# Optimization experiments

Measured on AMD Instinct MI355X. Metric: run time of the kernel, lower is better.

## Reference

```python
import jax, jax.numpy as jnp
import numpy as np


def setup_inputs() -> dict:
    key = jax.random.key(0)
    ks = jax.random.split(key, 10)
    N1, N2, F, D, E = 50000, 50000, 1024, 128, 1000000
    s = 0.02
    return {
        "x_gene": jax.random.normal(ks[0], (N1, F), jnp.float32),
        "x_cell": jax.random.normal(ks[1], (N2, F), jnp.float32),
        "edge_label_index": jax.random.randint(ks[2], (2, E), 0, N1, jnp.int64 if jax.config.jax_enable_x64 else jnp.int32),
        "W1": jax.random.normal(ks[3], (F, D), jnp.float32) * s,
        "b1": jnp.zeros((D,), jnp.float32),
        "W2": jax.random.normal(ks[4], (F, D), jnp.float32) * s,
        "b2": jnp.zeros((D,), jnp.float32),
        "Wm1": jax.random.normal(ks[5], (2 * D, 64), jnp.float32) * s,
        "bm1": jnp.zeros((64,), jnp.float32),
        "Wm2": jax.random.normal(ks[6], (64, 32), jnp.float32) * s,
        "bm2": jnp.zeros((32,), jnp.float32),
        "Wm3": jax.random.normal(ks[7], (32, 1), jnp.float32) * s,
        "bm3": jnp.zeros((1,), jnp.float32),
    }


def reference(x_gene, x_cell, edge_label_index, W1, b1, W2, b2, Wm1, bm1, Wm2, bm2, Wm3, bm3):
    # Node-type linear projections (dropout is identity in eval mode)
    h1 = x_gene @ W1 + b1          # [N1, D]
    h2 = x_cell @ W2 + b2          # [N2, D]
    # Edge gather + concat
    ef = jnp.concatenate([h1[edge_label_index[0]], h2[edge_label_index[1]]], axis=-1)  # [E, 2D]
    # 3-layer MLP classifier
    h = jax.nn.relu(ef @ Wm1 + bm1)
    h = jax.nn.relu(h @ Wm2 + bm2)
    pred = (h @ Wm3 + bm3)[..., 0]  # squeeze(-1) -> [E]
    return pred
```

## Files before the change

### kernel.cpp

```cpp
#include <hip/hip_runtime.h>
#include <hip/hip_bf16.h>
#include <stdint.h>

typedef __attribute__((ext_vector_type(8))) short short8;
typedef __attribute__((ext_vector_type(4))) float float4v;

__device__ __forceinline__ float bf2f(uint16_t u) {
    union { uint32_t i; float f; } v; v.i = ((uint32_t)u) << 16; return v.f;
}
__device__ __forceinline__ uint16_t f2bf(float f) {
    union { float f; uint32_t i; } v; v.f = f;
    uint32_t x = v.i;
    uint32_t r = (x + 0x7fffu + ((x >> 16) & 1u)) >> 16;
    return (uint16_t)r;
}

__global__ __launch_bounds__(256) void precompute_kernel(
    const float* __restrict__ W1, const float* __restrict__ W2,
    const float* __restrict__ Wm1, const float* __restrict__ Wm2,
    const float* __restrict__ b1, const float* __restrict__ b2,
    const float* __restrict__ bm1,
    uint16_t* __restrict__ A1T, uint16_t* __restrict__ A2T,
    float* __restrict__ tbias, uint16_t* __restrict__ Wm2bfT)
{
    int b = blockIdx.x, t = threadIdx.x;
    if (b < 512) {
        int g   = b * 4 + (t >> 6);
        int mat = g >> 10;
        int f   = g & 1023;
        int n   = t & 63;
        const float* W    = mat ? W2 : W1;
        const float* wm   = Wm1 + mat * 128 * 64;
        const float* Wrow = W + (size_t)f * 128;
        float acc = 0.f;
        #pragma unroll 8
        for (int d = 0; d < 128; ++d)
            acc = fmaf(Wrow[d], wm[d * 64 + n], acc);
        (mat ? A2T : A1T)[(size_t)n * 1024 + f] = f2bf(acc);
    } else {
        int n  = t >> 3;
        int k0 = (t & 7) * 8;
        #pragma unroll
        for (int i = 0; i < 8; ++i)
            Wm2bfT[n * 64 + k0 + i] = f2bf(Wm2[(size_t)(k0 + i) * 32 + n]);
        if (t < 64) {
            float acc = bm1[t];
            for (int d = 0; d < 128; ++d) acc += b1[d] * Wm1[d * 64 + t];
            for (int d = 0; d < 128; ++d) acc += b2[d] * Wm1[(128 + d) * 64 + t];
            tbias[t] = acc;
        }
    }
}

__global__ __launch_bounds__(256) void gemm64_kernel(
    const float* __restrict__ X1, const float* __restrict__ X2,
    const uint16_t* __restrict__ A1T, const uint16_t* __restrict__ A2T,
    uint16_t* __restrict__ G1, uint16_t* __restrict__ G2, int M1, int M2)
{
    const int which = blockIdx.y;
    const float* __restrict__ X     = which ? X2  : X1;
    const uint16_t* __restrict__ BT = which ? A2T : A1T;
    uint16_t* __restrict__ G        = which ? G2  : G1;
    const int M = which ? M2 : M1;

    const int blockRow = blockIdx.x * 64;
    if (blockRow >= M) return;

    __shared__ uint16_t As[64 * 128];

    const int t    = threadIdx.x;
    const int wid  = t >> 6;
    const int lane = t & 63;
    const int m    = lane & 15;
    const int q    = lane >> 4;

    float4v acc[4];
    #pragma unroll
    for (int nt = 0; nt < 4; ++nt) acc[nt] = (float4v){0.f, 0.f, 0.f, 0.f};

    for (int kk = 0; kk < 8; ++kk) {
        float4 av0[4], av1[4];
        int    dstc[4];
        #pragma unroll
        for (int it = 0; it < 4; ++it) {
            int c   = it * 256 + t;
            int row = c >> 4, pc = c & 15;
            int lc  = pc ^ (row & 7);
            int grow = blockRow + row; if (grow >= M) grow = M - 1;
            const float4* src = (const float4*)(X + (size_t)grow * 1024 + kk * 128 + lc * 8);
            av0[it] = src[0];
            av1[it] = src[1];
            dstc[it] = c * 8;
        }
        __syncthreads();
        #pragma unroll
        for (int it = 0; it < 4; ++it) {
            uint4 pk;
            pk.x = (uint32_t)f2bf(av0[it].x) | ((uint32_t)f2bf(av0[it].y) << 16);
            pk.y = (uint32_t)f2bf(av0[it].z) | ((uint32_t)f2bf(av0[it].w) << 16);
            pk.z = (uint32_t)f2bf(av1[it].x) | ((uint32_t)f2bf(av1[it].y) << 16);
            pk.w = (uint32_t)f2bf(av1[it].z) | ((uint32_t)f2bf(av1[it].w) << 16);
            *(uint4*)(As + dstc[it]) = pk;
        }
        __syncthreads();

        #pragma unroll
        for (int p = 0; p < 4; ++p) {
            short8 af, bfr[4];
            int row = wid * 16 + m;
            int pc  = (p * 4 + q) ^ (row & 7);
            af = *(const short8*)(As + row * 128 + pc * 8);
            #pragma unroll
            for (int nt = 0; nt < 4; ++nt) {
                int n = nt * 16 + m;
                bfr[nt] = *(const short8*)(BT + (size_t)n * 1024 + kk * 128 + (p * 4 + q) * 8);
            }
            #pragma unroll
            for (int nt = 0; nt < 4; ++nt)
                acc[nt] = __builtin_amdgcn_mfma_f32_16x16x32_bf16(
                    af, bfr[nt], acc[nt], 0, 0, 0);
        }
    }

    #pragma unroll
    for (int reg = 0; reg < 4; ++reg) {
        int grow = blockRow + wid * 16 + q * 4 + reg;
        if (grow < M) {
            #pragma unroll
            for (int nt = 0; nt < 4; ++nt)
                G[(size_t)grow * 64 + nt * 16 + m] = f2bf(acc[nt][reg]);
        }
    }
}

__global__ __launch_bounds__(256) void edge_mlp_kernel(
    const uint16_t* __restrict__ g1, const uint16_t* __restrict__ g2,
    const float* __restrict__ tbias, const int* __restrict__ eidx,
    const uint16_t* __restrict__ Wm2bfT, const float* __restrict__ bm2,
    const float* __restrict__ Wm3, const float* __restrict__ bm3,
    float* __restrict__ out, int E)
{
    __shared__ uint16_t T[256 * 64];

    const int t    = threadIdx.x;
    const int wid  = t >> 6;
    const int lane = t & 63;
    const int m    = lane & 15;
    const int q    = lane >> 4;

    short8 bfrag[2][2];
    #pragma unroll
    for (int s = 0; s < 2; ++s)
        #pragma unroll
        for (int nt = 0; nt < 2; ++nt)
            bfrag[s][nt] = *(const short8*)(Wm2bfT + (nt * 16 + m) * 64 + s * 32 + q * 8);

    const float bm2a = bm2[m],      bm2b = bm2[16 + m];
    const float w3a  = Wm3[m],      w3b  = Wm3[16 + m];
    const float b3   = bm3[0];

    const int tileBase = blockIdx.x * 256;
    int e = tileBase + t; if (e >= E) e = E - 1;
    const int src = eidx[e];
    const int dst = eidx[E + e];
    const uint4* r1 = (const uint4*)(g1 + (size_t)src * 64);
    const uint4* r2 = (const uint4*)(g2 + (size_t)dst * 64);

    uint4 A[8], B[8];
    #pragma unroll
    for (int c = 0; c < 8; ++c) { A[c] = r1[c]; B[c] = r2[c]; }

    #pragma unroll
    for (int c = 0; c < 8; ++c) {
        uint32_t aw[4] = { A[c].x, A[c].y, A[c].z, A[c].w };
        uint32_t bw[4] = { B[c].x, B[c].y, B[c].z, B[c].w };
        uint32_t pw[4];
        #pragma unroll
        for (int h = 0; h < 4; ++h) {
            float alo, ahi, blo, bhi;
            { union { uint32_t i; float f; } v; v.i = aw[h] << 16;        alo = v.f; }
            { union { uint32_t i; float f; } v; v.i = aw[h] & 0xffff0000u; ahi = v.f; }
            { union { uint32_t i; float f; } v; v.i = bw[h] << 16;        blo = v.f; }
            { union { uint32_t i; float f; } v; v.i = bw[h] & 0xffff0000u; bhi = v.f; }
            float t0 = fmaxf(alo + blo + tbias[c * 8 + 2 * h],     0.f);
            float t1 = fmaxf(ahi + bhi + tbias[c * 8 + 2 * h + 1], 0.f);
            pw[h] = (uint32_t)f2bf(t0) | ((uint32_t)f2bf(t1) << 16);
        }
        uint4 pk; pk.x = pw[0]; pk.y = pw[1]; pk.z = pw[2]; pk.w = pw[3];
        int pc = c ^ (t & 7);
        *(uint4*)(T + t * 64 + pc * 8) = pk;
    }
    __syncthreads();

    float4v acc[4][2];
    #pragma unroll
    for (int r = 0; r < 4; ++r) {
        acc[r][0] = (float4v){0.f, 0.f, 0.f, 0.f};
        acc[r][1] = (float4v){0.f, 0.f, 0.f, 0.f};
    }
    #pragma unroll
    for (int r = 0; r < 4; ++r) {
        const int row = wid * 64 + r * 16 + m;
        #pragma unroll
        for (int s = 0; s < 2; ++s) {
            const int pc = (s * 4 + q) ^ (row & 7);
            short8 af = *(const short8*)(T + row * 64 + pc * 8);
            acc[r][0] = __builtin_amdgcn_mfma_f32_16x16x32_bf16(af, bfrag[s][0], acc[r][0], 0, 0, 0);
            acc[r][1] = __builtin_amdgcn_mfma_f32_16x16x32_bf16(af, bfrag[s][1], acc[r][1], 0, 0, 0);
        }
    }

    #pragma unroll
    for (int r = 0; r < 4; ++r) {
        #pragma unroll
        for (int reg = 0; reg < 4; ++reg) {
            float v0 = fmaxf(acc[r][0][reg] + bm2a, 0.f);
            float v1 = fmaxf(acc[r][1][reg] + bm2b, 0.f);
            float p  = fmaf(v0, w3a, v1 * w3b);
            p += __shfl_xor(p, 1);
            p += __shfl_xor(p, 2);
            p += __shfl_xor(p, 4);
            p += __shfl_xor(p, 8);
            int eo = tileBase + wid * 64 + r * 16 + q * 4 + reg;
            if (m == 0 && eo < E) out[eo] = p + b3;
        }
    }
}

extern "C" void kernel_launch(void* const* d_in, const int* in_sizes, int n_in,
                              void* d_out, int out_size, void* d_ws, size_t ws_size,
                              hipStream_t stream) {
    const float* x_gene = (const float*)d_in[0];
    const float* x_cell = (const float*)d_in[1];
    const int*   eidx   = (const int*)d_in[2];
    const float* W1  = (const float*)d_in[3];
    const float* b1  = (const float*)d_in[4];
    const float* W2  = (const float*)d_in[5];
    const float* b2  = (const float*)d_in[6];
    const float* Wm1 = (const float*)d_in[7];
    const float* bm1 = (const float*)d_in[8];
    const float* Wm2 = (const float*)d_in[9];
    const float* bm2 = (const float*)d_in[10];
    const float* Wm3 = (const float*)d_in[11];
    const float* bm3 = (const float*)d_in[12];

    const int M1 = in_sizes[0] / 1024;
    const int M2 = in_sizes[1] / 1024;
    const int E  = in_sizes[2] / 2;

    uint8_t* ws = (uint8_t*)d_ws;
    uint16_t* A1T    = (uint16_t*)(ws + 0);
    uint16_t* A2T    = (uint16_t*)(ws + 131072);
    float*    tbias  = (float*)(ws + 262144);
    uint16_t* Wm2bfT = (uint16_t*)(ws + 262400);
    uint16_t* G1     = (uint16_t*)(ws + 524288);
    size_t g1_bytes  = ((size_t)M1 * 64 * 2 + 127) & ~(size_t)127;
    uint16_t* G2     = (uint16_t*)(ws + 524288 + g1_bytes);

    precompute_kernel<<<513, 256, 0, stream>>>(
        W1, W2, Wm1, Wm2, b1, b2, bm1, A1T, A2T, tbias, Wm2bfT);

    int Mmax = M1 > M2 ? M1 : M2;
    dim3 ggrid((Mmax + 63) / 64, 2);
    gemm64_kernel<<<ggrid, 256, 0, stream>>>(x_gene, x_cell, A1T, A2T, G1, G2, M1, M2);

    edge_mlp_kernel<<<(E + 255) / 256, 256, 0, stream>>>(
        G1, G2, tbias, eidx, Wm2bfT, bm2, Wm3, bm3, (float*)d_out, E);
}
```

Before: 543.6 us.

## Pipeline GEMM input loads with async global-to-LDS triple buffering

```diff
diff --git a/kernel.cpp b/kernel.cpp
--- a/kernel.cpp
+++ b/kernel.cpp
@@ -5,9 +5,9 @@
 typedef __attribute__((ext_vector_type(8))) short short8;
 typedef __attribute__((ext_vector_type(4))) float float4v;
 
-__device__ __forceinline__ float bf2f(uint16_t u) {
-    union { uint32_t i; float f; } v; v.i = ((uint32_t)u) << 16; return v.f;
-}
+typedef const __attribute__((address_space(1))) uint32_t* gas_ptr;
+typedef __attribute__((address_space(3))) uint32_t*       las_ptr;
+
 __device__ __forceinline__ uint16_t f2bf(float f) {
     union { float f; uint32_t i; } v; v.f = f;
     uint32_t x = v.i;
@@ -52,7 +52,7 @@
     }
 }
 
-__global__ __launch_bounds__(256) void gemm64_kernel(
+__global__ __launch_bounds__(256, 3) void gemm64_kernel(
     const float* __restrict__ X1, const float* __restrict__ X2,
     const uint16_t* __restrict__ A1T, const uint16_t* __restrict__ A2T,
     uint16_t* __restrict__ G1, uint16_t* __restrict__ G2, int M1, int M2)
@@ -66,61 +66,94 @@
     const int blockRow = blockIdx.x * 64;
     if (blockRow >= M) return;
 
-    __shared__ uint16_t As[64 * 128];
+    __shared__ __align__(16) float As[3 * 64 * 64];
 
     const int t    = threadIdx.x;
     const int wid  = t >> 6;
     const int lane = t & 63;
     const int m    = lane & 15;
     const int q    = lane >> 4;
+    const int sblk = wid * 4;
+
+    const float *sa0, *sa1, *sa2, *sa3;
+    {
+        int r0 = (sblk + 0) * 4 + (lane >> 4);
+        int r1 = (sblk + 1) * 4 + (lane >> 4);
+        int r2 = (sblk + 2) * 4 + (lane >> 4);
+        int r3 = (sblk + 3) * 4 + (lane >> 4);
+        int g0 = blockRow + r0; if (g0 >= M) g0 = M - 1;
+        int g1 = blockRow + r1; if (g1 >= M) g1 = M - 1;
+        int g2 = blockRow + r2; if (g2 >= M) g2 = M - 1;
+        int g3 = blockRow + r3; if (g3 >= M) g3 = M - 1;
+        sa0 = X + (size_t)g0 * 1024 + (((lane & 15) ^ (r0 & 15)) * 4);
+        sa1 = X + (size_t)g1 * 1024 + (((lane & 15) ^ (r1 & 15)) * 4);
+        sa2 = X + (size_t)g2 * 1024 + (((lane & 15) ^ (r2 & 15)) * 4);
+        sa3 = X + (size_t)g3 * 1024 + (((lane & 15) ^ (r3 & 15)) * 4);
+    }
+
+#define STAGE(ii, tb)                                                          \
+    do {                                                                       \
+        __builtin_amdgcn_global_load_lds((gas_ptr)(sa0 + (ii) * 64),           \
+            (las_ptr)((tb) + (sblk + 0) * 256), 16, 0, 0);                     \
+        __builtin_amdgcn_global_load_lds((gas_ptr)(sa1 + (ii) * 64),           \
+            (las_ptr)((tb) + (sblk + 1) * 256), 16, 0, 0);                     \
+        __builtin_amdgcn_global_load_lds((gas_ptr)(sa2 + (ii) * 64),           \
+            (las_ptr)((tb) + (sblk + 2) * 256), 16, 0, 0);                     \
+        __builtin_amdgcn_global_load_lds((gas_ptr)(sa3 + (ii) * 64),           \
+            (las_ptr)((tb) + (sblk + 3) * 256), 16, 0, 0);                     \
+    } while (0)
 
     float4v acc[4];
     #pragma unroll
     for (int nt = 0; nt < 4; ++nt) acc[nt] = (float4v){0.f, 0.f, 0.f, 0.f};
 
-    for (int kk = 0; kk < 8; ++kk) {
-        float4 av0[4], av1[4];
-        int    dstc[4];
-        #pragma unroll
-        for (int it = 0; it < 4; ++it) {
-            int c   = it * 256 + t;
-            int row = c >> 4, pc = c & 15;
-            int lc  = pc ^ (row & 7);
-            int grow = blockRow + row; if (grow >= M) grow = M - 1;
-            const float4* src = (const float4*)(X + (size_t)grow * 1024 + kk * 128 + lc * 8);
-            av0[it] = src[0];
-            av1[it] = src[1];
-            dstc[it] = c * 8;
-        }
-        __syncthreads();
-        #pragma unroll
-        for (int it = 0; it < 4; ++it) {
-            uint4 pk;
-            pk.x = (uint32_t)f2bf(av0[it].x) | ((uint32_t)f2bf(av0[it].y) << 16);
-            pk.y = (uint32_t)f2bf(av0[it].z) | ((uint32_t)f2bf(av0[it].w) << 16);
-            pk.z = (uint32_t)f2bf(av1[it].x) | ((uint32_t)f2bf(av1[it].y) << 16);
-            pk.w = (uint32_t)f2bf(av1[it].z) | ((uint32_t)f2bf(av1[it].w) << 16);
-            *(uint4*)(As + dstc[it]) = pk;
-        }
-        __syncthreads();
-
-        #pragma unroll
-        for (int p = 0; p < 4; ++p) {
-            short8 af, bfr[4];
-            int row = wid * 16 + m;
-            int pc  = (p * 4 + q) ^ (row & 7);
-            af = *(const short8*)(As + row * 128 + pc * 8);
+    STAGE(0, As);
+    STAGE(1, As + 4096);
+
+    const int row = wid * 16 + m;
+    const int hx  = row & 15;
+
+    #pragma unroll
+    for (int i = 0; i < 16; ++i) {
+        short8 bfr[2][4];
+        #pragma unroll
+        for (int s = 0; s < 2; ++s)
             #pragma unroll
-            for (int nt = 0; nt < 4; ++nt) {
-                int n = nt * 16 + m;
-                bfr[nt] = *(const short8*)(BT + (size_t)n * 1024 + kk * 128 + (p * 4 + q) * 8);
-            }
+            for (int nt = 0; nt < 4; ++nt)
+                bfr[s][nt] = *(const short8*)(
+                    BT + (size_t)(nt * 16 + m) * 1024 + i * 64 + (s * 4 + q) * 8);
+        __builtin_amdgcn_sched_barrier(0);
+
+        __builtin_amdgcn_s_barrier();
+        if (i + 2 < 16) {
+            float* tb_next = As + ((i + 2) % 3) * 4096;
+            STAGE(i + 2, tb_next);
+        }
+        if (i < 14)       asm volatile("s_waitcnt vmcnt(16)" ::: "memory");
+        else if (i == 14) asm volatile("s_waitcnt vmcnt(12)" ::: "memory");
+        else              asm volatile("s_waitcnt vmcnt(8)"  ::: "memory");
+        __builtin_amdgcn_sched_barrier(0);
+        __builtin_amdgcn_s_barrier();
+        __builtin_amdgcn_sched_barrier(0);
+
+        const float*  tb = As + (i % 3) * 4096;
+        const float4* t4 = (const float4*)tb + row * 16;
+        #pragma unroll
+        for (int s = 0; s < 2; ++s) {
+            float4 x0 = t4[(2 * (s * 4 + q))     ^ hx];
+            float4 x1 = t4[(2 * (s * 4 + q) + 1) ^ hx];
+            union { short8 s8; uint32_t u[4]; } P;
+            P.u[0] = (uint32_t)f2bf(x0.x) | ((uint32_t)f2bf(x0.y) << 16);
+            P.u[1] = (uint32_t)f2bf(x0.z) | ((uint32_t)f2bf(x0.w) << 16);
+            P.u[2] = (uint32_t)f2bf(x1.x) | ((uint32_t)f2bf(x1.y) << 16);
+            P.u[3] = (uint32_t)f2bf(x1.z) | ((uint32_t)f2bf(x1.w) << 16);
             #pragma unroll
             for (int nt = 0; nt < 4; ++nt)
                 acc[nt] = __builtin_amdgcn_mfma_f32_16x16x32_bf16(
-                    af, bfr[nt], acc[nt], 0, 0, 0);
-        }
-    }
+                    P.s8, bfr[s][nt], acc[nt], 0, 0, 0);
+        }
+    }
+#undef STAGE
 
     #pragma unroll
     for (int reg = 0; reg < 4; ++reg) {
```

New measurement: 531.1 us. 2.3% less time.
